# Kernel optimization log

Measured on AMD Instinct MI355X. Metric: run time of the kernel, lower is better.

The kernel has to match this reference:

```python
import jax, jax.numpy as jnp
import numpy as np


def _pool_mat(N, pn):
    # F.interpolate(mode='area') == adaptive_avg_pool1d: output i averages
    # input indices [floor(i*N/pn), ceil((i+1)*N/pn))
    W = np.zeros((pn, N), dtype=np.float32)
    for i in range(pn):
        s = (i * N) // pn
        e = -((-(i + 1) * N) // pn)  # ceil((i+1)*N/pn)
        W[i, s:e] = 1.0 / (e - s)
    return W


def _up_mat(pn, N):
    # F.interpolate(mode='linear', align_corners=False) from length pn to N
    W = np.zeros((N, pn), dtype=np.float32)
    scale = pn / N
    for j in range(N):
        pos = max((j + 0.5) * scale - 0.5, 0.0)
        i0 = min(int(np.floor(pos)), pn - 1)
        i1 = min(i0 + 1, pn - 1)
        frac = pos - i0
        W[j, i0] += 1.0 - frac
        W[j, i1] += frac
    return W


def setup_inputs() -> dict:
    key = jax.random.key(0)
    k1, k2 = jax.random.split(key)
    B, N, C, K = 512, 16, 256, 8192
    f = jax.random.normal(k1, (B, N, C), dtype=jnp.float32)
    # original init: uniform(-1/K, 1/K)
    emb = jax.random.uniform(k2, (K, C), dtype=jnp.float32, minval=-1.0 / K, maxval=1.0 / K)
    return {"f": f, "emb": emb}


def reference(f, emb):
    B, N, C = f.shape
    fT = jnp.transpose(f, (0, 2, 1))            # [B, C, N]
    f_ng = jax.lax.stop_gradient(fT)
    emb_ng = jax.lax.stop_gradient(emb)
    e_sq = jnp.sum(emb_ng * emb_ng, axis=1)     # [K]
    f_rest = f_ng
    f_hat = jnp.zeros_like(f_ng)
    commit = jnp.float32(0.0)
    qlat = jnp.float32(0.0)
    for pn in range(1, N + 1):
        rest_bcn = jax.lax.stop_gradient(f_rest)
        if pn < N:
            Wp = jnp.asarray(_pool_mat(N, pn))             # [pn, N]
            rest = jnp.einsum('pn,bcn->bpc', Wp, rest_bcn).reshape(-1, C)
        else:
            rest = jnp.transpose(rest_bcn, (0, 2, 1)).reshape(-1, C)
        # squared euclidean distances [B*pn, K]
        d = jnp.sum(rest * rest, axis=1, keepdims=True) + e_sq - 2.0 * (rest @ emb_ng.T)
        idx = jnp.argmin(d, axis=1).reshape(B, pn)
        h = jnp.transpose(emb[idx], (0, 2, 1))             # [B, C, pn]
        if pn < N:
            Wu = jnp.asarray(_up_mat(pn, N))               # [N, pn]
            h = jnp.einsum('np,bcp->bcn', Wu, h)
        f_hat = f_hat + h
        f_rest = f_rest - h
        commit = commit + 0.25 * jnp.mean((jax.lax.stop_gradient(f_hat) - fT) ** 2)
        qlat = qlat + jnp.mean((f_hat - f_ng) ** 2)
    commit = commit / N
    qlat = qlat / N
    # straight-through estimator
    f_hat_out = jax.lax.stop_gradient(f_hat) - f_ng + fT
    return jnp.transpose(f_hat_out, (0, 2, 1)), commit, qlat
```

## Files before the change

kernel.cpp:

```cpp
#include <hip/hip_runtime.h>
#include <math.h>

#define BB 512
#define NN 16
#define CC 256
#define KK 8192
#define BNC (BB*NN*CC)

typedef unsigned short u16;
typedef __attribute__((ext_vector_type(8))) short bf16x8;
typedef __attribute__((ext_vector_type(4))) float f32x4;

__device__ __forceinline__ u16 f2bf(float x) {
    unsigned u = __float_as_uint(x);
    unsigned r = (u + 0x7fffu + ((u >> 16) & 1u)) >> 16;
    return (u16)r;
}

__device__ __forceinline__ void gl2lds16(const void* g, void* l) {
    __builtin_amdgcn_global_load_lds(
        (const __attribute__((address_space(1))) void*)g,
        (__attribute__((address_space(3))) void*)l,
        16, 0, 0);
}

__global__ void esq_kernel(const float* __restrict__ emb, float* __restrict__ e_sq) {
    int gid  = blockIdx.x * blockDim.x + threadIdx.x;
    int wave = gid >> 6;
    int lane = gid & 63;
    const float4 v = *(const float4*)(emb + (size_t)wave * CC + lane * 4);
    float s = v.x*v.x + v.y*v.y + v.z*v.z + v.w*v.w;
    #pragma unroll
    for (int m = 32; m >= 1; m >>= 1) s += __shfl_xor(s, m, 64);
    if (lane == 0) e_sq[wave] = s;
}

__global__ void cvt_emb_kernel(const float* __restrict__ emb, u16* __restrict__ out) {
    int gid = blockIdx.x * blockDim.x + threadIdx.x;
    float4 v = ((const float4*)emb)[gid];
    ushort4 o;
    o.x = f2bf(v.x); o.y = f2bf(v.y); o.z = f2bf(v.z); o.w = f2bf(v.w);
    ((ushort4*)out)[gid] = o;
}

__global__ void init_pool_kernel(const float* __restrict__ f,
                                 u16* __restrict__ rest_bf) {
    int b = blockIdx.x;
    int c = threadIdx.x;
    const float* base = f + (size_t)b * NN * CC + c;
    float acc = 0.f;
    #pragma unroll
    for (int n = 0; n < NN; ++n) acc += base[(size_t)n * CC];
    rest_bf[(size_t)b * CC + c] = f2bf(acc * (1.0f / 16.0f));
}

__device__ __forceinline__ unsigned long long shfl_xor_u64(unsigned long long v, int m) {
    unsigned lo = (unsigned)v, hi = (unsigned)(v >> 32);
    lo = __shfl_xor(lo, m, 64);
    hi = __shfl_xor(hi, m, 64);
    return ((unsigned long long)hi << 32) | lo;
}

__global__ __launch_bounds__(256, 2) void dist_mfma_kernel(
        const u16* __restrict__ A, const u16* __restrict__ Bm,
        const float* __restrict__ e_sq,
        unsigned long long* __restrict__ packed, int cpb) {
    __shared__ __align__(16) u16 sA[16384];
    __shared__ __align__(16) u16 sB[16384];
    const int tid = threadIdx.x;
    const int w = tid >> 6, l = tid & 63;
    const int r0 = blockIdx.x * 64;
    const int c0 = blockIdx.y * cpb;
    const int ncb = cpb >> 8;
    const int arow = l & 15;
    const int aq   = l >> 4;

    {
        const int phys = tid & 31;
        #pragma unroll
        for (int i = 0; i < 8; ++i) {
            int s = tid + 256 * i;
            int row = s >> 5;
            int g = phys ^ (row & 31);
            gl2lds16(A + (((size_t)(r0 + row)) << 8) + g * 8,
                     (char*)sA + (size_t)(w * 64 + 256 * i) * 16);
        }
    }
    const int gsel = (l & 3) ^ ((l >> 2) & 3) ^ ((l >> 4) & 3);
    const int crow = l >> 2;

    #define STAGE_B(cb_, kc_, buf_)                                            \
        {                                                                      \
            const u16* src = Bm + (((size_t)(c0 + (cb_) * 256 + w * 64)) << 8) \
                             + (kc_) * 32 + gsel * 8;                          \
            char* dst = (char*)sB + ((w * 2 + (buf_)) << 12);                  \
            _Pragma("unroll")                                                  \
            for (int ld = 0; ld < 4; ++ld)                                     \
                gl2lds16(src + ((size_t)(crow + 16 * ld) << 8), dst + (ld << 10)); \
        }

    STAGE_B(0, 0, 0);
    __syncthreads();

    float bestd[16];
    int   bestk[16];
    #pragma unroll
    for (int t = 0; t < 16; ++t) { bestd[t] = 1e30f; bestk[t] = 0; }

    for (int cb = 0; cb < ncb; ++cb) {
        f32x4 acc[4][4];
        const f32x4 z = {0.f, 0.f, 0.f, 0.f};
        #pragma unroll
        for (int i = 0; i < 4; ++i)
            #pragma unroll
            for (int j = 0; j < 4; ++j) acc[i][j] = z;

        #pragma unroll
        for (int kc = 0; kc < 8; ++kc) {
            const int buf = kc & 1;
            __builtin_amdgcn_s_waitcnt(0x0F70);
            bf16x8 a[4], b[4];
            const u16* wb = sB + ((w * 2 + buf) << 11);
            #pragma unroll
            for (int t = 0; t < 4; ++t) {
                int row = t * 16 + arow;
                int g = kc * 4 + aq;
                int phys = g ^ (row & 31);
                a[t] = *(const bf16x8*)(sA + row * 256 + phys * 8);
                int cc_ = t * 16 + arow;
                int sig = cc_ * 4 + (aq ^ (cc_ & 3) ^ ((cc_ >> 2) & 3));
                b[t] = *(const bf16x8*)(wb + sig * 8);
            }
            int cbn = (kc == 7) ? ((cb + 1 < ncb) ? cb + 1 : cb) : cb;
            int kcn = (kc + 1) & 7;
            STAGE_B(cbn, kcn, buf ^ 1);
            #pragma unroll
            for (int i = 0; i < 4; ++i)
                #pragma unroll
                for (int j = 0; j < 4; ++j)
                    acc[i][j] = __builtin_amdgcn_mfma_f32_16x16x32_bf16(
                                    a[i], b[j], acc[i][j], 0, 0, 0);
        }

        float esq[4];
        #pragma unroll
        for (int j = 0; j < 4; ++j)
            esq[j] = e_sq[c0 + cb * 256 + w * 64 + j * 16 + arow];
        #pragma unroll
        for (int i = 0; i < 4; ++i)
            #pragma unroll
            for (int r = 0; r < 4; ++r) {
                const int slot = i * 4 + r;
                #pragma unroll
                for (int j = 0; j < 4; ++j) {
                    float d = fmaf(-2.0f, acc[i][j][r], esq[j]);
                    int k = c0 + cb * 256 + w * 64 + j * 16 + arow;
                    if (d < bestd[slot]) { bestd[slot] = d; bestk[slot] = k; }
                }
            }
    }

    #pragma unroll
    for (int t = 0; t < 16; ++t) {
        unsigned u = __float_as_uint(bestd[t]);
        u = (u & 0x80000000u) ? ~u : (u | 0x80000000u);
        unsigned long long p = ((unsigned long long)u << 32) | (unsigned)bestk[t];
        #pragma unroll
        for (int m = 1; m < 16; m <<= 1) {
            unsigned long long o = shfl_xor_u64(p, m);
            if (o < p) p = o;
        }
        if (arow == 0)
            atomicMin(&packed[r0 + (t >> 2) * 16 + aq * 4 + (t & 3)], p);
    }
    #undef STAGE_B
}

__global__ void update_pool_kernel(const float* __restrict__ f,
                                   const float* __restrict__ emb,
                                   const unsigned long long* __restrict__ packed,
                                   float* __restrict__ f_rest,
                                   float* __restrict__ f_hat,
                                   float* __restrict__ slots,
                                   u16* __restrict__ rest_bf, int pn) {
    int b = blockIdx.x;
    int c = threadIdx.x;
    __shared__ int sk[NN];
    __shared__ float red[4];
    if (threadIdx.x < pn)
        sk[threadIdx.x] = (int)(unsigned)(packed[b * pn + threadIdx.x] & 0xffffffffull);
    __syncthreads();

    float fr[NN];
    float acc_sq = 0.f;
    #pragma unroll
    for (int n = 0; n < NN; ++n) {
        double pos = (n + 0.5) * ((double)pn / 16.0) - 0.5;
        if (pos < 0.0) pos = 0.0;
        int i0 = (int)floor(pos);
        if (i0 > pn - 1) i0 = pn - 1;
        int i1 = i0 + 1;
        if (i1 > pn - 1) i1 = pn - 1;
        double frac = pos - (double)i0;
        float w1 = (float)frac;
        float w0 = (float)(1.0 - frac);
        float h = w0 * emb[(size_t)sk[i0] * CC + c] + w1 * emb[(size_t)sk[i1] * CC + c];
        size_t off = ((size_t)b * NN + n) * CC + c;
        float fh = f_hat[off] + h;
        f_hat[off] = fh;
        float fre = f_rest[off] - h;
        f_rest[off] = fre;
        fr[n] = fre;
        float diff = fh - f[off];
        acc_sq += diff * diff;
    }

    int wv = threadIdx.x >> 6, ln = threadIdx.x & 63;
    #pragma unroll
    for (int m = 32; m >= 1; m >>= 1) acc_sq += __shfl_xor(acc_sq, m, 64);
    if (ln == 0) red[wv] = acc_sq;

    int pn2 = pn + 1;
    if (pn < NN) {
        for (int p = 0; p < pn2; ++p) {
            int s = (p * NN) / pn2;
            int e = ((p + 1) * NN + pn2 - 1) / pn2;
            float v = 0.f;
            for (int n = s; n < e; ++n) v += fr[n];
            v *= 1.0f / (float)(e - s);
            rest_bf[((size_t)(b * pn2 + p)) * CC + c] = f2bf(v);
        }
    }
    __syncthreads();
    if (threadIdx.x == 0)
        atomicAdd(&slots[b & 255], (red[0] + red[1]) + (red[2] + red[3]));
}

__global__ void final_kernel(const float* __restrict__ slots, float* __restrict__ out_scalars) {
    float v = slots[threadIdx.x];
    #pragma unroll
    for (int m = 32; m >= 1; m >>= 1) v += __shfl_xor(v, m, 64);
    __shared__ float red[4];
    int wv = threadIdx.x >> 6, ln = threadIdx.x & 63;
    if (ln == 0) red[wv] = v;
    __syncthreads();
    if (threadIdx.x == 0) {
        float S = (red[0] + red[1]) + (red[2] + red[3]);
        float qlat = S / (float)BNC / (float)NN;
        out_scalars[0] = 0.25f * qlat;
        out_scalars[1] = qlat;
    }
}

extern "C" void kernel_launch(void* const* d_in, const int* in_sizes, int n_in,
                              void* d_out, int out_size, void* d_ws, size_t ws_size,
                              hipStream_t stream) {
    (void)in_sizes; (void)n_in; (void)out_size; (void)ws_size;
    const float* f   = (const float*)d_in[0];
    const float* emb = (const float*)d_in[1];
    float* out = (float*)d_out;

    float* ws      = (float*)d_ws;
    float* f_rest  = ws;
    float* r2_pad  = f_rest + BNC;
    float* e_sq    = r2_pad + BB * NN;
    float* slots   = e_sq + KK;
    unsigned long long* packed_all = (unsigned long long*)(slots + 256);
    u16* rest_bf = (u16*)(packed_all + (size_t)BB * 136);
    u16* emb_bf  = rest_bf + (size_t)BB * NN * CC;

    float* f_hat = out;

    hipMemsetAsync(out, 0, (size_t)BNC * sizeof(float), stream);
    hipMemcpyAsync(f_rest, f, (size_t)BNC * sizeof(float), hipMemcpyDeviceToDevice, stream);
    hipMemsetAsync(slots, 0, 256 * sizeof(float), stream);
    hipMemsetAsync(packed_all, 0xFF, (size_t)BB * 136 * sizeof(unsigned long long), stream);
    esq_kernel<<<KK / 4, 256, 0, stream>>>(emb, e_sq);
    cvt_emb_kernel<<<KK * CC / 4 / 256, 256, 0, stream>>>(emb, emb_bf);
    init_pool_kernel<<<BB, 256, 0, stream>>>(f, rest_bf);

    static const int splits_tab[17] = {0,32,32,16,16,8,8,8,8,4,4,4,4,4,4,4,4};

    for (int pn = 1; pn <= NN; ++pn) {
        unsigned long long* packed = packed_all + (size_t)BB * (pn * (pn - 1) / 2);
        int splits = splits_tab[pn];
        int cpb = KK / splits;
        dim3 grid(BB * pn / 64, splits);
        dist_mfma_kernel<<<grid, 256, 0, stream>>>(rest_bf, emb_bf, e_sq, packed, cpb);
        update_pool_kernel<<<BB, 256, 0, stream>>>(f, emb, packed, f_rest, f_hat,
                                                   slots, rest_bf, pn);
    }
    final_kernel<<<1, 256, 0, stream>>>(slots, out + BNC);
}
```

Measured before the change: 819.1 us.

## Load codebook fragments directly to registers and fold norm into MFMA accumulator

The codebook B operand is no longer staged through shared memory with global_load_lds. Each lane now loads its bf16 fragments straight from global memory into a 4-deep register ring, prefetching three k-steps ahead, which removes the sB buffer and the waitcnt. The distance calculation is also folded into the GEMM: the codebook is negated at conversion, e_sq is halved, and the accumulators start at 0.5*e_sq, so the epilogue compares accumulators directly with no fma. Costs are extra VGPR pressure from the 16 fragment registers and uncoalesced 16-byte global loads spread across rows, which rely on L2 hits.

```diff
diff --git a/kernel.cpp b/kernel.cpp
--- a/kernel.cpp
+++ b/kernel.cpp
@@ -32,14 +32,14 @@
     float s = v.x*v.x + v.y*v.y + v.z*v.z + v.w*v.w;
     #pragma unroll
     for (int m = 32; m >= 1; m >>= 1) s += __shfl_xor(s, m, 64);
-    if (lane == 0) e_sq[wave] = s;
+    if (lane == 0) e_sq[wave] = 0.5f * s;
 }
 
 __global__ void cvt_emb_kernel(const float* __restrict__ emb, u16* __restrict__ out) {
     int gid = blockIdx.x * blockDim.x + threadIdx.x;
     float4 v = ((const float4*)emb)[gid];
     ushort4 o;
-    o.x = f2bf(v.x); o.y = f2bf(v.y); o.z = f2bf(v.z); o.w = f2bf(v.w);
+    o.x = f2bf(-v.x); o.y = f2bf(-v.y); o.z = f2bf(-v.z); o.w = f2bf(-v.w);
     ((ushort4*)out)[gid] = o;
 }
 
@@ -66,7 +66,6 @@
         const float* __restrict__ e_sq,
         unsigned long long* __restrict__ packed, int cpb) {
     __shared__ __align__(16) u16 sA[16384];
-    __shared__ __align__(16) u16 sB[16384];
     const int tid = threadIdx.x;
     const int w = tid >> 6, l = tid & 63;
     const int r0 = blockIdx.x * 64;
@@ -86,66 +85,68 @@
                      (char*)sA + (size_t)(w * 64 + 256 * i) * 16);
         }
     }
-    const int gsel = (l & 3) ^ ((l >> 2) & 3) ^ ((l >> 4) & 3);
-    const int crow = l >> 2;
-
-    #define STAGE_B(cb_, kc_, buf_)                                            \
-        {                                                                      \
-            const u16* src = Bm + (((size_t)(c0 + (cb_) * 256 + w * 64)) << 8) \
-                             + (kc_) * 32 + gsel * 8;                          \
-            char* dst = (char*)sB + ((w * 2 + (buf_)) << 12);                  \
-            _Pragma("unroll")                                                  \
-            for (int ld = 0; ld < 4; ++ld)                                     \
-                gl2lds16(src + ((size_t)(crow + 16 * ld) << 8), dst + (ld << 10)); \
-        }
-
-    STAGE_B(0, 0, 0);
-    __syncthreads();
+
+    const u16* bbase = Bm + (((size_t)(c0 + w * 64 + arow)) << 8) + aq * 8;
+    const float* eb = e_sq + c0 + w * 64 + arow;
+    const int tmax = ncb * 8 - 1;
+
+    bf16x8 b[4][4];
+    #define LOADB(buf_, t_) {                                                   \
+        const u16* p_ = bbase + (((size_t)((t_) >> 3)) << 16) + (((t_) & 7) << 5); \
+        b[buf_][0] = *(const bf16x8*)(p_);                                      \
+        b[buf_][1] = *(const bf16x8*)(p_ + 4096);                               \
+        b[buf_][2] = *(const bf16x8*)(p_ + 8192);                               \
+        b[buf_][3] = *(const bf16x8*)(p_ + 12288); }
+
+    LOADB(0, 0)
+    LOADB(1, 1)
+    LOADB(2, 2)
+
+    float eq[4];
+    #pragma unroll
+    for (int j = 0; j < 4; ++j) eq[j] = eb[j * 16];
 
     float bestd[16];
     int   bestk[16];
     #pragma unroll
     for (int t = 0; t < 16; ++t) { bestd[t] = 1e30f; bestk[t] = 0; }
 
+    __syncthreads();
+
     for (int cb = 0; cb < ncb; ++cb) {
         f32x4 acc[4][4];
-        const f32x4 z = {0.f, 0.f, 0.f, 0.f};
-        #pragma unroll
-        for (int i = 0; i < 4; ++i)
-            #pragma unroll
-            for (int j = 0; j < 4; ++j) acc[i][j] = z;
-
+        #pragma unroll
+        for (int j = 0; j < 4; ++j) {
+            const f32x4 e = {eq[j], eq[j], eq[j], eq[j]};
+            #pragma unroll
+            for (int i = 0; i < 4; ++i) acc[i][j] = e;
+        }
+        if (cb + 1 < ncb) {
+            #pragma unroll
+            for (int j = 0; j < 4; ++j) eq[j] = eb[(cb + 1) * 256 + j * 16];
+        }
+
+        const int tb = cb * 8;
         #pragma unroll
         for (int kc = 0; kc < 8; ++kc) {
-            const int buf = kc & 1;
-            __builtin_amdgcn_s_waitcnt(0x0F70);
-            bf16x8 a[4], b[4];
-            const u16* wb = sB + ((w * 2 + buf) << 11);
+            bf16x8 a[4];
             #pragma unroll
             for (int t = 0; t < 4; ++t) {
-                int row = t * 16 + arow;
-                int g = kc * 4 + aq;
-                int phys = g ^ (row & 31);
+                const int row = t * 16 + arow;
+                const int phys = (kc * 4 + aq) ^ (row & 31);
                 a[t] = *(const bf16x8*)(sA + row * 256 + phys * 8);
-                int cc_ = t * 16 + arow;
-                int sig = cc_ * 4 + (aq ^ (cc_ & 3) ^ ((cc_ >> 2) & 3));
-                b[t] = *(const bf16x8*)(wb + sig * 8);
             }
-            int cbn = (kc == 7) ? ((cb + 1 < ncb) ? cb + 1 : cb) : cb;
-            int kcn = (kc + 1) & 7;
-            STAGE_B(cbn, kcn, buf ^ 1);
+            int tp = tb + kc + 3;
+            if (tp > tmax) tp = tmax;
+            LOADB((kc + 3) & 3, tp)
             #pragma unroll
             for (int i = 0; i < 4; ++i)
                 #pragma unroll
                 for (int j = 0; j < 4; ++j)
                     acc[i][j] = __builtin_amdgcn_mfma_f32_16x16x32_bf16(
-                                    a[i], b[j], acc[i][j], 0, 0, 0);
-        }
-
-        float esq[4];
-        #pragma unroll
-        for (int j = 0; j < 4; ++j)
-            esq[j] = e_sq[c0 + cb * 256 + w * 64 + j * 16 + arow];
+                                    a[i], b[kc & 3][j], acc[i][j], 0, 0, 0);
+        }
+
         #pragma unroll
         for (int i = 0; i < 4; ++i)
             #pragma unroll
@@ -153,12 +154,13 @@
                 const int slot = i * 4 + r;
                 #pragma unroll
                 for (int j = 0; j < 4; ++j) {
-                    float d = fmaf(-2.0f, acc[i][j][r], esq[j]);
-                    int k = c0 + cb * 256 + w * 64 + j * 16 + arow;
+                    const float d = acc[i][j][r];
+                    const int k = c0 + cb * 256 + w * 64 + j * 16 + arow;
                     if (d < bestd[slot]) { bestd[slot] = d; bestk[slot] = k; }
                 }
             }
     }
+    #undef LOADB
 
     #pragma unroll
     for (int t = 0; t < 16; ++t) {
@@ -173,7 +175,6 @@
         if (arow == 0)
             atomicMin(&packed[r0 + (t >> 2) * 16 + aq * 4 + (t & 3)], p);
     }
-    #undef STAGE_B
 }
 
 __global__ void update_pool_kernel(const float* __restrict__ f,
```

Result: slower. 1.354 ms (+65.3%).
